# Kernel tuning notes

Measured on AMD Instinct MI355X. Metric: run time of the kernel, lower is better.

The kernel has to match this reference:

```python
import jax, jax.numpy as jnp
import numpy as np

N, E, B = 60000, 360000, 64        # nodes, edges, graphs
IN_DIM, HID, L, NCLS = 256, 512, 3, 1000
EPS = 1e-5                          # BatchNorm1d eps


def setup_inputs() -> dict:
    key = jax.random.key(0)
    ks = jax.random.split(key, 10)
    s = 0.05
    x = jax.random.normal(ks[0], (N, IN_DIM), dtype=jnp.float32)
    edge_index = jax.random.randint(ks[1], (2, E), 0, N, dtype=jnp.int32)
    batch = jnp.sort(jax.random.randint(ks[2], (N,), 0, B, dtype=jnp.int32))
    W_embed = jax.random.normal(ks[3], (IN_DIM, HID), dtype=jnp.float32) * s
    # per-block params (all 3 blocks have identical shapes -> stacked on axis 0)
    W1 = jax.random.normal(ks[4], (L, 2 * HID, HID), dtype=jnp.float32) * s
    b1 = jnp.zeros((L, HID), jnp.float32)
    g1 = jnp.ones((L, HID), jnp.float32)
    be1 = jnp.zeros((L, HID), jnp.float32)
    W2 = jax.random.normal(ks[5], (L, 2 * HID, HID), dtype=jnp.float32) * s
    b2 = jnp.zeros((L, HID), jnp.float32)
    g2 = jnp.ones((L, HID), jnp.float32)
    be2 = jnp.zeros((L, HID), jnp.float32)
    W_att = jax.random.normal(ks[6], (HID, 1), dtype=jnp.float32) * s
    W_read = jax.random.normal(ks[7], (HID, NCLS), dtype=jnp.float32) * s
    return dict(x=x, edge_index=edge_index, batch=batch, W_embed=W_embed,
                W1=W1, b1=b1, g1=g1, be1=be1, W2=W2, b2=b2, g2=g2, be2=be2,
                W_att=W_att, W_read=W_read)


def _segment_mean(vals, idx, num):
    s = jax.ops.segment_sum(vals, idx, num_segments=num)
    c = jax.ops.segment_sum(jnp.ones((vals.shape[0], 1), vals.dtype), idx, num_segments=num)
    return s / jnp.maximum(c, 1.0)


def _bn(h, g, b):  # BatchNorm1d, training-mode batch statistics (biased var)
    m = h.mean(0)
    v = jnp.mean((h - m) ** 2, axis=0)
    return (h - m) * jax.lax.rsqrt(v + EPS) * g + b


def _sage(h, src, dst, W, b):
    # MySAGEConv (position=False -> message = x_j), aggr='mean', concat=True, L2 normalize
    aggr = _segment_mean(h[src], dst, h.shape[0])          # [N, d] mean of neighbor msgs
    out = jnp.concatenate([h, aggr], axis=-1) @ W + b      # [N, 2d] @ [2d, d]
    norm = jnp.linalg.norm(out, axis=-1, keepdims=True)
    return out / jnp.maximum(norm, 1e-12)                  # F.normalize(p=2)


def reference(x, edge_index, batch, W_embed, W1, b1, g1, be1,
              W2, b2, g2, be2, W_att, W_read):
    src, dst = edge_index[0], edge_index[1]
    h = x @ W_embed
    for l in range(L):  # MySAGEConvBlock, gcn_num=2, has_linear_in_block=False
        identity = h
        out = jax.nn.relu(_bn(_sage(h, src, dst, W1[l], b1[l]), g1[l], be1[l]))
        out = jax.nn.relu(_bn(_sage(out, src, dst, W2[l], b2[l]), g2[l], be2[l]))
        h = out + identity  # residual (dims match)
    # AttentionClass
    att = jax.nn.sigmoid(h @ W_att)           # [N, 1]
    hx = (att * h + h) * 0.5
    hg = _segment_mean(hx, batch, B)          # global mean pool per graph
    return hg @ W_read                        # [B, 1000] logits
```

## Files before the change

kernel.cpp:

```cpp
#include <hip/hip_runtime.h>
#include <math.h>

#define N_NODES 60000
#define N_EDGES 360000
#define N_GRAPH 64
#define HID 512
#define NCLS 1000
#define BN_EPS 1e-5f
#define NS ((size_t)N_NODES * HID)
#define NB 235

typedef __bf16 bf16x8 __attribute__((ext_vector_type(8)));
typedef float f32x4 __attribute__((ext_vector_type(4)));

static __device__ __forceinline__ unsigned short f2bf(float f) {
  unsigned u = __float_as_uint(f);
  unsigned r = (u + 0x7fffu + ((u >> 16) & 1u)) >> 16;
  return (unsigned short)r;
}
static __device__ __forceinline__ float bfLo(unsigned u) { return __uint_as_float(u << 16); }
static __device__ __forceinline__ float bfHi(unsigned u) { return __uint_as_float(u & 0xffff0000u); }
static __device__ __forceinline__ unsigned packbf(float a, float b) {
  return (unsigned)f2bf(a) | ((unsigned)f2bf(b) << 16);
}

__global__ void write_sentinel(float* out, float v) { out[0] = v; }

__global__ __launch_bounds__(256) void wtrans(const float* __restrict__ W,
                                              unsigned short* __restrict__ Wt,
                                              int K, int N) {
  __shared__ float sh[32][33];
  int kt = blockIdx.x * 32, nt = blockIdx.y * 32;
  int tx = threadIdx.x & 31, ty = threadIdx.x >> 5;
#pragma unroll
  for (int i = 0; i < 4; ++i)
    sh[ty + i * 8][tx] = W[(size_t)(kt + ty + i * 8) * N + nt + tx];
  __syncthreads();
#pragma unroll
  for (int i = 0; i < 4; ++i)
    Wt[(size_t)(nt + ty + i * 8) * K + kt + tx] = f2bf(sh[tx][ty + i * 8]);
}

__global__ __launch_bounds__(256) void count_deg(const int* __restrict__ dst,
                                                 int* __restrict__ deg, int E) {
  int e = blockIdx.x * 256 + threadIdx.x;
  if (e < E) atomicAdd(&deg[dst[e]], 1);
}

__global__ __launch_bounds__(256) void make_invdeg(const int* __restrict__ deg,
                                                   float* __restrict__ inv, int n) {
  int i = blockIdx.x * 256 + threadIdx.x;
  if (i < n) inv[i] = 1.0f / fmaxf((float)deg[i], 1.0f);
}

__global__ __launch_bounds__(256) void scan_part(const int* __restrict__ deg,
                                                 int* __restrict__ bsum, int n) {
  __shared__ int sh[256];
  int i = blockIdx.x * 256 + threadIdx.x;
  sh[threadIdx.x] = (i < n) ? deg[i] : 0;
  __syncthreads();
  for (int off = 128; off; off >>= 1) {
    if (threadIdx.x < off) sh[threadIdx.x] += sh[threadIdx.x + off];
    __syncthreads();
  }
  if (threadIdx.x == 0) bsum[blockIdx.x] = sh[0];
}

__global__ __launch_bounds__(256) void scan_bsums(int* __restrict__ bsum, int nb) {
  __shared__ int sh[256];
  int t = threadIdx.x;
  int v = (t < nb) ? bsum[t] : 0;
  sh[t] = v;
  __syncthreads();
  for (int off = 1; off < 256; off <<= 1) {
    int u = (t >= off) ? sh[t - off] : 0;
    __syncthreads();
    sh[t] += u;
    __syncthreads();
  }
  if (t < nb) bsum[t] = sh[t] - v;
}

__global__ __launch_bounds__(256) void scan_final(const int* __restrict__ deg,
                                                  const int* __restrict__ bsum,
                                                  int* __restrict__ rowptr, int n) {
  __shared__ int sh[256];
  int t = threadIdx.x;
  int i = blockIdx.x * 256 + t;
  int v = (i < n) ? deg[i] : 0;
  sh[t] = v;
  __syncthreads();
  for (int off = 1; off < 256; off <<= 1) {
    int u = (t >= off) ? sh[t - off] : 0;
    __syncthreads();
    sh[t] += u;
    __syncthreads();
  }
  if (i < n) rowptr[i + 1] = bsum[blockIdx.x] + sh[t];
  if (i == 0) rowptr[0] = 0;
}

__global__ __launch_bounds__(256) void fill_csr(const int* __restrict__ src,
                                                const int* __restrict__ dst,
                                                const int* __restrict__ rowptr,
                                                int* __restrict__ fillc,
                                                int* __restrict__ esrc, int E) {
  int e = blockIdx.x * 256 + threadIdx.x;
  if (e < E) {
    int d = dst[e];
    int pos = rowptr[d] + atomicAdd(&fillc[d], 1);
    esrc[pos] = src[e];
  }
}

__global__ __launch_bounds__(256) void bcount(const int* __restrict__ batch,
                                              float* __restrict__ bcnt, int n) {
  __shared__ int h[N_GRAPH];
  if (threadIdx.x < N_GRAPH) h[threadIdx.x] = 0;
  __syncthreads();
  int i = blockIdx.x * 256 + threadIdx.x;
  if (i < n) atomicAdd(&h[batch[i]], 1);
  __syncthreads();
  if (threadIdx.x < N_GRAPH && h[threadIdx.x])
    atomicAdd(&bcnt[threadIdx.x], (float)h[threadIdx.x]);
}

__global__ __launch_bounds__(256) void gemm_glds(
    const unsigned short* __restrict__ Xb, int ldx,
    const unsigned short* __restrict__ Wt, int ldw,
    const float* __restrict__ bias,
    unsigned short* __restrict__ outB, int M) {
  __shared__ __align__(16) unsigned short As[128 * 32];
  __shared__ __align__(16) unsigned short Bs[128 * 32];
  const int tid = threadIdx.x;
  const int bm = blockIdx.x * 128;
  const int bn = blockIdx.y * 128;
  const int wv = tid >> 6, lane = tid & 63;
  const int wm = (wv >> 1) * 64, wn = (wv & 1) * 64;
  const int lm = lane & 15, quad = lane >> 4;
  const int crow = lane >> 2, cseg = (lane & 3) * 8;

  f32x4 zero;
  zero[0] = 0.f; zero[1] = 0.f; zero[2] = 0.f; zero[3] = 0.f;
  f32x4 acc[4][4];
#pragma unroll
  for (int i = 0; i < 4; ++i)
#pragma unroll
    for (int j = 0; j < 4; ++j) acc[i][j] = zero;

  for (int kt = 0; kt < 512; kt += 32) {
    __syncthreads();
#pragma unroll
    for (int r = 0; r < 2; ++r) {
      int chunk = wv + r * 4;
      int row = chunk * 16 + crow;
      const unsigned short* ga = Xb + (size_t)(bm + row) * ldx + kt + cseg;
      const unsigned short* gb = Wt + (size_t)(bn + row) * ldw + kt + cseg;
      __builtin_amdgcn_global_load_lds(
          (const __attribute__((address_space(1))) unsigned int*)ga,
          (__attribute__((address_space(3))) unsigned int*)(As + chunk * 512),
          16, 0, 0);
      __builtin_amdgcn_global_load_lds(
          (const __attribute__((address_space(1))) unsigned int*)gb,
          (__attribute__((address_space(3))) unsigned int*)(Bs + chunk * 512),
          16, 0, 0);
    }
    __syncthreads();
    bf16x8 af[4], bfr[4];
#pragma unroll
    for (int i = 0; i < 4; ++i)
      af[i] = *(const bf16x8*)(As + (wm + i * 16 + lm) * 32 + quad * 8);
#pragma unroll
    for (int j = 0; j < 4; ++j)
      bfr[j] = *(const bf16x8*)(Bs + (wn + j * 16 + lm) * 32 + quad * 8);
#pragma unroll
    for (int i = 0; i < 4; ++i)
#pragma unroll
      for (int j = 0; j < 4; ++j)
        acc[i][j] = __builtin_amdgcn_mfma_f32_16x16x32_bf16(af[i], bfr[j], acc[i][j], 0, 0, 0);
  }

  const int qr = quad * 4;
#pragma unroll
  for (int j = 0; j < 4; ++j) {
    int col = bn + wn + j * 16 + lm;
    float bvv = bias ? bias[col] : 0.f;
#pragma unroll
    for (int i = 0; i < 4; ++i) {
      int rbase = bm + wm + i * 16 + qr;
#pragma unroll
      for (int r = 0; r < 4; ++r) {
        int row = rbase + r;
        if (row < M) outB[(size_t)row * 512 + col] = f2bf(acc[i][j][r] + bvv);
      }
    }
  }
}

__global__ __launch_bounds__(256) void gemm_tiled(
    const float* __restrict__ Xf, int ldx, int K,
    const unsigned short* __restrict__ Wt, int ldw,
    const float* __restrict__ bias,
    unsigned short* __restrict__ outB, int M) {
  __shared__ __align__(16) unsigned short As[128][40];
  __shared__ __align__(16) unsigned short Bs[128][40];
  const int tid = threadIdx.x;
  const int bm = blockIdx.x * 128;
  const int bn = blockIdx.y * 128;
  const int wv = tid >> 6, lane = tid & 63;
  const int wm = (wv >> 1) * 64, wn = (wv & 1) * 64;
  const int lm = lane & 15, quad = lane >> 4, lk = quad * 8;
  const int srow = tid >> 2, sseg = (tid & 3) * 8;

  f32x4 zero;
  zero[0] = 0.f; zero[1] = 0.f; zero[2] = 0.f; zero[3] = 0.f;
  f32x4 acc[4][4];
#pragma unroll
  for (int i = 0; i < 4; ++i)
#pragma unroll
    for (int j = 0; j < 4; ++j) acc[i][j] = zero;

  const int r0 = bm + srow, r1 = bm + 64 + srow;
  for (int kt = 0; kt < K; kt += 32) {
    uint4 a0 = make_uint4(0, 0, 0, 0), a1 = make_uint4(0, 0, 0, 0);
    if (r0 < M) {
      const float* xp = Xf + (size_t)r0 * ldx + kt + sseg;
      float4 f0 = *(const float4*)xp, f1 = *(const float4*)(xp + 4);
      a0.x = packbf(f0.x, f0.y); a0.y = packbf(f0.z, f0.w);
      a0.z = packbf(f1.x, f1.y); a0.w = packbf(f1.z, f1.w);
    }
    if (r1 < M) {
      const float* xp = Xf + (size_t)r1 * ldx + kt + sseg;
      float4 f0 = *(const float4*)xp, f1 = *(const float4*)(xp + 4);
      a1.x = packbf(f0.x, f0.y); a1.y = packbf(f0.z, f0.w);
      a1.z = packbf(f1.x, f1.y); a1.w = packbf(f1.z, f1.w);
    }
    uint4 b0 = *(const uint4*)(Wt + (size_t)(bn + srow) * ldw + kt + sseg);
    uint4 b1 = *(const uint4*)(Wt + (size_t)(bn + 64 + srow) * ldw + kt + sseg);
    __syncthreads();
    *(uint4*)(&As[srow][sseg]) = a0;
    *(uint4*)(&As[srow + 64][sseg]) = a1;
    *(uint4*)(&Bs[srow][sseg]) = b0;
    *(uint4*)(&Bs[srow + 64][sseg]) = b1;
    __syncthreads();
    bf16x8 af[4], bfr[4];
#pragma unroll
    for (int i = 0; i < 4; ++i) af[i] = *(const bf16x8*)(&As[wm + i * 16 + lm][lk]);
#pragma unroll
    for (int j = 0; j < 4; ++j) bfr[j] = *(const bf16x8*)(&Bs[wn + j * 16 + lm][lk]);
#pragma unroll
    for (int i = 0; i < 4; ++i)
#pragma unroll
      for (int j = 0; j < 4; ++j)
        acc[i][j] = __builtin_amdgcn_mfma_f32_16x16x32_bf16(af[i], bfr[j], acc[i][j], 0, 0, 0);
  }

  const int qr = quad * 4;
#pragma unroll
  for (int j = 0; j < 4; ++j) {
    int col = bn + wn + j * 16 + lm;
    float bvv = bias ? bias[col] : 0.f;
#pragma unroll
    for (int i = 0; i < 4; ++i) {
      int rbase = bm + wm + i * 16 + qr;
#pragma unroll
      for (int r = 0; r < 4; ++r) {
        int row = rbase + r;
        if (row < M) outB[(size_t)row * 512 + col] = f2bf(acc[i][j][r] + bvv);
      }
    }
  }
}

__global__ __launch_bounds__(512) void gemm_strip(
    const unsigned short* __restrict__ Xb, int ldx,
    const unsigned short* __restrict__ Wt, int ldw,
    const float* __restrict__ bias,
    unsigned short* __restrict__ outB, int M) {
  __shared__ __align__(16) unsigned short As[64][40];
  const int tid = threadIdx.x;
  const int bm = blockIdx.x * 64;
  const int wv = tid >> 6, lane = tid & 63;
  const int lm = lane & 15, quad = lane >> 4, lk = quad * 8;
  const int cb = wv * 64;
  const int arow = tid >> 3, aseg = (tid & 7) * 4;

  f32x4 zero;
  zero[0] = 0.f; zero[1] = 0.f; zero[2] = 0.f; zero[3] = 0.f;
  f32x4 acc[4][4];
#pragma unroll
  for (int i = 0; i < 4; ++i)
#pragma unroll
    for (int j = 0; j < 4; ++j) acc[i][j] = zero;

  for (int kt = 0; kt < 512; kt += 32) {
    uint2 av = make_uint2(0, 0);
    int gr = bm + arow;
    if (gr < M) av = *(const uint2*)(Xb + (size_t)gr * ldx + kt + aseg);
    bf16x8 bfr[4];
#pragma unroll
    for (int j = 0; j < 4; ++j)
      bfr[j] = *(const bf16x8*)(Wt + (size_t)(cb + j * 16 + lm) * ldw + kt + lk);
    __syncthreads();
    *(uint2*)(&As[arow][aseg]) = av;
    __syncthreads();
    bf16x8 af[4];
#pragma unroll
    for (int i = 0; i < 4; ++i) af[i] = *(const bf16x8*)(&As[i * 16 + lm][lk]);
#pragma unroll
    for (int i = 0; i < 4; ++i)
#pragma unroll
      for (int j = 0; j < 4; ++j)
        acc[i][j] = __builtin_amdgcn_mfma_f32_16x16x32_bf16(af[i], bfr[j], acc[i][j], 0, 0, 0);
  }

  const int qr = quad * 4;
#pragma unroll
  for (int j = 0; j < 4; ++j) {
    int col = cb + j * 16 + lm;
    float bvv = bias ? bias[col] : 0.f;
#pragma unroll
    for (int i = 0; i < 4; ++i) {
      int rbase = bm + i * 16 + qr;
#pragma unroll
      for (int r = 0; r < 4; ++r) {
        int row = rbase + r;
        if (row < M) outB[(size_t)row * 512 + col] = f2bf(acc[i][j][r] + bvv);
      }
    }
  }
}

__global__ __launch_bounds__(256) void aggr_norm(
    unsigned short* __restrict__ Ya, const unsigned short* __restrict__ Yb,
    const int* __restrict__ rowptr, const int* __restrict__ esrc,
    const float* __restrict__ invdeg, int M) {
  int d = blockIdx.x * 4 + (threadIdx.x >> 6);
  int lane = threadIdx.x & 63;
  if (d >= M) return;
  float acc[8] = {0.f, 0.f, 0.f, 0.f, 0.f, 0.f, 0.f, 0.f};
  int beg = rowptr[d], end = rowptr[d + 1];
  for (int e = beg; e < end; ++e) {
    int s = esrc[e];
    uint4 u = *(const uint4*)(Yb + (size_t)s * 512 + lane * 8);
    acc[0] += bfLo(u.x); acc[1] += bfHi(u.x);
    acc[2] += bfLo(u.y); acc[3] += bfHi(u.y);
    acc[4] += bfLo(u.z); acc[5] += bfHi(u.z);
    acc[6] += bfLo(u.w); acc[7] += bfHi(u.w);
  }
  float iv = invdeg[d];
  uint4 a = *(const uint4*)(Ya + (size_t)d * 512 + lane * 8);
  float r0 = bfLo(a.x) + iv * acc[0], r1 = bfHi(a.x) + iv * acc[1];
  float r2 = bfLo(a.y) + iv * acc[2], r3 = bfHi(a.y) + iv * acc[3];
  float r4 = bfLo(a.z) + iv * acc[4], r5 = bfHi(a.z) + iv * acc[5];
  float r6 = bfLo(a.w) + iv * acc[6], r7 = bfHi(a.w) + iv * acc[7];
  float ss = r0 * r0 + r1 * r1 + r2 * r2 + r3 * r3
           + r4 * r4 + r5 * r5 + r6 * r6 + r7 * r7;
#pragma unroll
  for (int o = 32; o; o >>= 1) ss += __shfl_xor(ss, o, 64);
  float inv = 1.0f / fmaxf(sqrtf(ss), 1e-12f);
  uint4 o4;
  o4.x = packbf(r0 * inv, r1 * inv);
  o4.y = packbf(r2 * inv, r3 * inv);
  o4.z = packbf(r4 * inv, r5 * inv);
  o4.w = packbf(r6 * inv, r7 * inv);
  *(uint4*)(Ya + (size_t)d * 512 + lane * 8) = o4;
}

__global__ __launch_bounds__(256) void bn_stats(const unsigned short* __restrict__ T,
                                                int M, float* __restrict__ sums) {
  const int t = threadIdx.x;
  int r0 = blockIdx.x * 128;
  int rend = min(r0 + 128, M);
  float s0 = 0.f, q0 = 0.f, s1 = 0.f, q1 = 0.f;
  for (int r = r0; r < rend; ++r) {
    float a = __uint_as_float((unsigned)T[(size_t)r * 512 + t] << 16);
    float b = __uint_as_float((unsigned)T[(size_t)r * 512 + t + 256] << 16);
    s0 += a; q0 += a * a; s1 += b; q1 += b * b;
  }
  atomicAdd(&sums[t], s0);
  atomicAdd(&sums[t + 256], s1);
  atomicAdd(&sums[512 + t], q0);
  atomicAdd(&sums[512 + t + 256], q1);
}

__global__ __launch_bounds__(256) void bn_apply(const unsigned short* __restrict__ U,
                                                unsigned short* __restrict__ H,
                                                const float* __restrict__ sums,
                                                const float* __restrict__ g,
                                                const float* __restrict__ be,
                                                int M, int residual) {
  size_t i2 = (size_t)blockIdx.x * 256 + threadIdx.x;
  if (i2 >= NS / 2) return;
  int c = ((int)(i2 & 255)) * 2;
  float invM = 1.0f / (float)M;
  float m0 = sums[c] * invM, m1 = sums[c + 1] * invM;
  float v0 = sums[512 + c] * invM - m0 * m0;
  float v1 = sums[512 + c + 1] * invM - m1 * m1;
  float k0 = rsqrtf(v0 + BN_EPS) * g[c], k1 = rsqrtf(v1 + BN_EPS) * g[c + 1];
  unsigned u = ((const unsigned*)U)[i2];
  float x0 = fmaxf((bfLo(u) - m0) * k0 + be[c], 0.f);
  float x1 = fmaxf((bfHi(u) - m1) * k1 + be[c + 1], 0.f);
  if (residual) {
    unsigned hv = ((const unsigned*)H)[i2];
    x0 += bfLo(hv);
    x1 += bfHi(hv);
  }
  ((unsigned*)H)[i2] = packbf(x0, x1);
}

#define NPB 64
__global__ __launch_bounds__(256) void att_pool2(const unsigned short* __restrict__ H,
                                                 const int* __restrict__ batch,
                                                 const float* __restrict__ Watt,
                                                 float* __restrict__ hg, int M) {
  __shared__ float fsh[NPB];
  __shared__ int bsh[NPB];
  const int tid = threadIdx.x;
  const int base = blockIdx.x * NPB;
  if (tid < NPB) bsh[tid] = (base + tid < M) ? batch[base + tid] : -1;
  const int wv = tid >> 6, lane = tid & 63;
  float4 wa0 = *(const float4*)(Watt + lane * 8);
  float4 wa1 = *(const float4*)(Watt + lane * 8 + 4);
  __syncthreads();
  for (int i = wv; i < NPB; i += 4) {
    int node = base + i;
    float dot = 0.f;
    if (node < M) {
      uint4 u = *(const uint4*)(H + (size_t)node * 512 + lane * 8);
      dot = bfLo(u.x) * wa0.x + bfHi(u.x) * wa0.y
          + bfLo(u.y) * wa0.z + bfHi(u.y) * wa0.w
          + bfLo(u.z) * wa1.x + bfHi(u.z) * wa1.y
          + bfLo(u.w) * wa1.z + bfHi(u.w) * wa1.w;
    }
#pragma unroll
    for (int o = 32; o; o >>= 1) dot += __shfl_xor(dot, o, 64);
    if (lane == 0) fsh[i] = 0.5f * (1.0f + 1.0f / (1.0f + expf(-dot)));
  }
  __syncthreads();
  float a0 = 0.f, a1 = 0.f;
  int cur = bsh[0];
  for (int i = 0; i < NPB; ++i) {
    int node = base + i;
    if (node >= M) break;
    int b = bsh[i];
    if (b != cur) {
      atomicAdd(&hg[(size_t)cur * 512 + tid * 2], a0);
      atomicAdd(&hg[(size_t)cur * 512 + tid * 2 + 1], a1);
      a0 = a1 = 0.f;
      cur = b;
    }
    unsigned u = *(const unsigned*)(H + (size_t)node * 512 + tid * 2);
    float f = fsh[i];
    a0 += bfLo(u) * f;
    a1 += bfHi(u) * f;
  }
  if (cur >= 0) {
    atomicAdd(&hg[(size_t)cur * 512 + tid * 2], a0);
    atomicAdd(&hg[(size_t)cur * 512 + tid * 2 + 1], a1);
  }
}

__global__ __launch_bounds__(256) void readout(const float* __restrict__ hg,
                                               const float* __restrict__ bcnt,
                                               const float* __restrict__ Wr,
                                               float* __restrict__ out) {
  __shared__ float sh[HID];
  int g = blockIdx.x;
  int n = blockIdx.y * 256 + threadIdx.x;
  float inv = 1.0f / fmaxf(bcnt[g], 1.0f);
  for (int k = threadIdx.x; k < HID; k += 256) sh[k] = hg[(size_t)g * HID + k] * inv;
  __syncthreads();
  if (n < NCLS) {
    float acc = 0.f;
    for (int k = 0; k < HID; ++k) acc += sh[k] * Wr[(size_t)k * NCLS + n];
    out[(size_t)g * NCLS + n] = acc;
  }
}

extern "C" void kernel_launch(void* const* d_in, const int* in_sizes, int n_in,
                              void* d_out, int out_size, void* d_ws, size_t ws_size,
                              hipStream_t stream) {
  const float* x       = (const float*)d_in[0];
  const int*   ei      = (const int*)d_in[1];
  const int*   batch   = (const int*)d_in[2];
  const float* W_embed = (const float*)d_in[3];
  const float* W1      = (const float*)d_in[4];
  const float* b1      = (const float*)d_in[5];
  const float* g1      = (const float*)d_in[6];
  const float* be1     = (const float*)d_in[7];
  const float* W2      = (const float*)d_in[8];
  const float* b2      = (const float*)d_in[9];
  const float* g2      = (const float*)d_in[10];
  const float* be2     = (const float*)d_in[11];
  const float* Watt    = (const float*)d_in[12];
  const float* Wread   = (const float*)d_in[13];
  float* out = (float*)d_out;

  const int* srcIdx = ei;
  const int* dstIdx = ei + N_EDGES;

  char* p = (char*)d_ws;
  unsigned short* B0 = (unsigned short*)p; p += NS * 2;
  unsigned short* B1 = (unsigned short*)p; p += NS * 2;
  unsigned short* B2 = (unsigned short*)p; p += NS * 2;
  unsigned short* WtE = (unsigned short*)p; p += (size_t)512 * 256 * 2;
  unsigned short* Wt1 = (unsigned short*)p; p += (size_t)3 * 512 * 1024 * 2;
  unsigned short* Wt2 = (unsigned short*)p; p += (size_t)3 * 512 * 1024 * 2;
  float* hg     = (float*)p; p += (size_t)N_GRAPH * HID * 4;
  float* sums   = (float*)p; p += 1024 * 4;
  float* invdeg = (float*)p; p += (size_t)N_NODES * 4;
  float* bcnt   = (float*)p; p += 256;
  int* deg      = (int*)p;   p += (size_t)N_NODES * 4;
  int* fillc    = (int*)p;   p += (size_t)N_NODES * 4;
  int* esrc     = (int*)p;   p += (size_t)N_EDGES * 4;
  int* rowptr   = (int*)p;   p += (size_t)(N_NODES + 1) * 4;
  int* bsum     = (int*)p;   p += (size_t)NB * 4;
  size_t need3 = (size_t)(p - (char*)d_ws);
  if (ws_size < need3) {
    write_sentinel<<<1, 1, 0, stream>>>(out, (float)need3);
    return;
  }
  unsigned short* B3 = nullptr;
  if (ws_size >= need3 + NS * 2) B3 = (unsigned short*)((char*)d_ws + need3);

  wtrans<<<dim3(8, 16), 256, 0, stream>>>(W_embed, WtE, 256, 512);
  for (int l = 0; l < 3; ++l) {
    wtrans<<<dim3(32, 16), 256, 0, stream>>>(W1 + (size_t)l * 1024 * 512,
                                             Wt1 + (size_t)l * 512 * 1024, 1024, 512);
    wtrans<<<dim3(32, 16), 256, 0, stream>>>(W2 + (size_t)l * 1024 * 512,
                                             Wt2 + (size_t)l * 512 * 1024, 1024, 512);
  }

  hipMemsetAsync(deg, 0, N_NODES * sizeof(int), stream);
  hipMemsetAsync(fillc, 0, N_NODES * sizeof(int), stream);
  count_deg<<<(N_EDGES + 255) / 256, 256, 0, stream>>>(dstIdx, deg, N_EDGES);
  make_invdeg<<<(N_NODES + 255) / 256, 256, 0, stream>>>(deg, invdeg, N_NODES);
  scan_part<<<NB, 256, 0, stream>>>(deg, bsum, N_NODES);
  scan_bsums<<<1, 256, 0, stream>>>(bsum, NB);
  scan_final<<<NB, 256, 0, stream>>>(deg, bsum, rowptr, N_NODES);
  fill_csr<<<(N_EDGES + 255) / 256, 256, 0, stream>>>(srcIdx, dstIdx, rowptr, fillc,
                                                      esrc, N_EDGES);

  const dim3 tgrid((N_NODES + 127) / 128, 4);
  const int sgrid = (N_NODES + 63) / 64;
  const int ngrid = (N_NODES + 3) / 4;
  const int egrid = (int)((NS / 2 + 255) / 256);

  gemm_tiled<<<tgrid, 256, 0, stream>>>(x, 256, 256, WtE, 256, nullptr, B0, N_NODES);

  for (int l = 0; l < 3; ++l) {
    const unsigned short* Wt1l = Wt1 + (size_t)l * 512 * 1024;
    const unsigned short* Wt2l = Wt2 + (size_t)l * 512 * 1024;
    gemm_glds<<<tgrid, 256, 0, stream>>>(B0, 512, Wt1l + 512, 1024,
                                         nullptr, B2, N_NODES);
    gemm_glds<<<tgrid, 256, 0, stream>>>(B0, 512, Wt1l, 1024,
                                         b1 + l * 512, B1, N_NODES);
    aggr_norm<<<ngrid, 256, 0, stream>>>(B1, B2, rowptr, esrc, invdeg, N_NODES);
    hipMemsetAsync(sums, 0, 1024 * sizeof(float), stream);
    bn_stats<<<(N_NODES + 127) / 128, 256, 0, stream>>>(B1, N_NODES, sums);
    bn_apply<<<egrid, 256, 0, stream>>>(B1, B1, sums, g1 + l * 512,
                                        be1 + l * 512, N_NODES, 0);
    gemm_glds<<<tgrid, 256, 0, stream>>>(B1, 512, Wt2l + 512, 1024,
                                         nullptr, B2, N_NODES);
    unsigned short* Ya2 = B3 ? B3 : B1;
    if (B3) {
      gemm_glds<<<tgrid, 256, 0, stream>>>(B1, 512, Wt2l, 1024,
                                           b2 + l * 512, B3, N_NODES);
    } else {
      gemm_strip<<<sgrid, 512, 0, stream>>>(B1, 512, Wt2l, 1024,
                                            b2 + l * 512, B1, N_NODES);
    }
    aggr_norm<<<ngrid, 256, 0, stream>>>(Ya2, B2, rowptr, esrc, invdeg, N_NODES);
    hipMemsetAsync(sums, 0, 1024 * sizeof(float), stream);
    bn_stats<<<(N_NODES + 127) / 128, 256, 0, stream>>>(Ya2, N_NODES, sums);
    bn_apply<<<egrid, 256, 0, stream>>>(Ya2, B0, sums, g2 + l * 512,
                                        be2 + l * 512, N_NODES, 1);
  }

  hipMemsetAsync(hg, 0, (size_t)N_GRAPH * HID * sizeof(float), stream);
  hipMemsetAsync(bcnt, 0, N_GRAPH * sizeof(float), stream);
  bcount<<<NB, 256, 0, stream>>>(batch, bcnt, N_NODES);
  att_pool2<<<(N_NODES + NPB - 1) / NPB, 256, 0, stream>>>(B0, batch, Watt, hg, N_NODES);
  readout<<<dim3(N_GRAPH, 4), 256, 0, stream>>>(hg, bcnt, Wread, out);
}
```

Before: 2.211 ms.

## Remap gemm_glds blocks per XCD, fix LDS fragment layout, stage output via LDS

Replaces the 2D grid of gemm_glds with a 1D grid that spreads contiguous 128-row strips across the eight XCDs, so the four column tiles of a strip share one XCD's L2. It changes the global_load_lds lane-to-row mapping so each 16-row chunk is stored in MFMA fragment order, letting each lane read its fragment as one contiguous 16-byte LDS access. The epilogue now stages bf16 results in an LDS tile and writes full 16-byte rows to global memory instead of scattered 2-byte stores. This adds LDS use and two extra barrier phases per block. The grid of 1888 blocks includes 12 idle blocks that return immediately, and the workspace threshold for B3 is made slightly stricter.

```diff
diff --git a/kernel.cpp b/kernel.cpp
--- a/kernel.cpp
+++ b/kernel.cpp
@@ -9,6 +9,7 @@
 #define BN_EPS 1e-5f
 #define NS ((size_t)N_NODES * HID)
 #define NB 235
+#define STRIPS 469
 
 typedef __bf16 bf16x8 __attribute__((ext_vector_type(8)));
 typedef float f32x4 __attribute__((ext_vector_type(4)));
@@ -132,13 +133,18 @@
     unsigned short* __restrict__ outB, int M) {
   __shared__ __align__(16) unsigned short As[128 * 32];
   __shared__ __align__(16) unsigned short Bs[128 * 32];
+  __shared__ __align__(16) unsigned short Cs[64][136];
   const int tid = threadIdx.x;
-  const int bm = blockIdx.x * 128;
-  const int bn = blockIdx.y * 128;
+  const int L = blockIdx.x;
+  const int xcd = L & 7, li = L >> 3;
+  const int strip = xcd * 59 + (li >> 2);
+  if (strip >= STRIPS) return;
+  const int bm = strip * 128;
+  const int bn = (li & 3) * 128;
   const int wv = tid >> 6, lane = tid & 63;
   const int wm = (wv >> 1) * 64, wn = (wv & 1) * 64;
   const int lm = lane & 15, quad = lane >> 4;
-  const int crow = lane >> 2, cseg = (lane & 3) * 8;
+  const int grow = lane & 15, gseg = (lane >> 4) * 8;
 
   f32x4 zero;
   zero[0] = 0.f; zero[1] = 0.f; zero[2] = 0.f; zero[3] = 0.f;
@@ -153,9 +159,9 @@
 #pragma unroll
     for (int r = 0; r < 2; ++r) {
       int chunk = wv + r * 4;
-      int row = chunk * 16 + crow;
-      const unsigned short* ga = Xb + (size_t)(bm + row) * ldx + kt + cseg;
-      const unsigned short* gb = Wt + (size_t)(bn + row) * ldw + kt + cseg;
+      int row = chunk * 16 + grow;
+      const unsigned short* ga = Xb + (size_t)(bm + row) * ldx + kt + gseg;
+      const unsigned short* gb = Wt + (size_t)(bn + row) * ldw + kt + gseg;
       __builtin_amdgcn_global_load_lds(
           (const __attribute__((address_space(1))) unsigned int*)ga,
           (__attribute__((address_space(3))) unsigned int*)(As + chunk * 512),
@@ -169,10 +175,10 @@
     bf16x8 af[4], bfr[4];
 #pragma unroll
     for (int i = 0; i < 4; ++i)
-      af[i] = *(const bf16x8*)(As + (wm + i * 16 + lm) * 32 + quad * 8);
+      af[i] = *(const bf16x8*)(As + (wm / 16 + i) * 512 + lane * 8);
 #pragma unroll
     for (int j = 0; j < 4; ++j)
-      bfr[j] = *(const bf16x8*)(Bs + (wn + j * 16 + lm) * 32 + quad * 8);
+      bfr[j] = *(const bf16x8*)(Bs + (wn / 16 + j) * 512 + lane * 8);
 #pragma unroll
     for (int i = 0; i < 4; ++i)
 #pragma unroll
@@ -181,18 +187,29 @@
   }
 
   const int qr = quad * 4;
-#pragma unroll
-  for (int j = 0; j < 4; ++j) {
-    int col = bn + wn + j * 16 + lm;
-    float bvv = bias ? bias[col] : 0.f;
-#pragma unroll
-    for (int i = 0; i < 4; ++i) {
-      int rbase = bm + wm + i * 16 + qr;
-#pragma unroll
-      for (int r = 0; r < 4; ++r) {
-        int row = rbase + r;
-        if (row < M) outB[(size_t)row * 512 + col] = f2bf(acc[i][j][r] + bvv);
+  const int rl = tid >> 4, seg = (tid & 15) * 8;
+#pragma unroll
+  for (int p = 0; p < 2; ++p) {
+    __syncthreads();
+    if ((wv >> 1) == p) {
+#pragma unroll
+      for (int j = 0; j < 4; ++j) {
+        int col = wn + j * 16 + lm;
+        float bvv = bias ? bias[bn + col] : 0.f;
+#pragma unroll
+        for (int i = 0; i < 4; ++i)
+#pragma unroll
+          for (int r = 0; r < 4; ++r)
+            Cs[i * 16 + qr + r][col] = f2bf(acc[i][j][r] + bvv);
       }
+    }
+    __syncthreads();
+#pragma unroll
+    for (int pass = 0; pass < 4; ++pass) {
+      int row = bm + p * 64 + pass * 16 + rl;
+      if (row < M)
+        *(uint4*)(outB + (size_t)row * 512 + bn + seg) =
+            *(const uint4*)(&Cs[pass * 16 + rl][seg]);
     }
   }
 }
@@ -522,7 +539,7 @@
     return;
   }
   unsigned short* B3 = nullptr;
-  if (ws_size >= need3 + NS * 2) B3 = (unsigned short*)((char*)d_ws + need3);
+  if (ws_size >= need3 + NS * 2 + 65536) B3 = (unsigned short*)((char*)d_ws + need3);
 
   wtrans<<<dim3(8, 16), 256, 0, stream>>>(W_embed, WtE, 256, 512);
   for (int l = 0; l < 3; ++l) {
@@ -542,6 +559,7 @@
   fill_csr<<<(N_EDGES + 255) / 256, 256, 0, stream>>>(srcIdx, dstIdx, rowptr, fillc,
                                                       esrc, N_EDGES);
 
+  const int ggrid = 8 * 59 * 4;
   const dim3 tgrid((N_NODES + 127) / 128, 4);
   const int sgrid = (N_NODES + 63) / 64;
   const int ngrid = (N_NODES + 3) / 4;
@@ -552,20 +570,20 @@
   for (int l = 0; l < 3; ++l) {
     const unsigned short* Wt1l = Wt1 + (size_t)l * 512 * 1024;
     const unsigned short* Wt2l = Wt2 + (size_t)l * 512 * 1024;
-    gemm_glds<<<tgrid, 256, 0, stream>>>(B0, 512, Wt1l + 512, 1024,
+    gemm_glds<<<ggrid, 256, 0, stream>>>(B0, 512, Wt1l + 512, 1024,
                                          nullptr, B2, N_NODES);
-    gemm_glds<<<tgrid, 256, 0, stream>>>(B0, 512, Wt1l, 1024,
+    gemm_glds<<<ggrid, 256, 0, stream>>>(B0, 512, Wt1l, 1024,
                                          b1 + l * 512, B1, N_NODES);
     aggr_norm<<<ngrid, 256, 0, stream>>>(B1, B2, rowptr, esrc, invdeg, N_NODES);
     hipMemsetAsync(sums, 0, 1024 * sizeof(float), stream);
     bn_stats<<<(N_NODES + 127) / 128, 256, 0, stream>>>(B1, N_NODES, sums);
     bn_apply<<<egrid, 256, 0, stream>>>(B1, B1, sums, g1 + l * 512,
                                         be1 + l * 512, N_NODES, 0);
-    gemm_glds<<<tgrid, 256, 0, stream>>>(B1, 512, Wt2l + 512, 1024,
+    gemm_glds<<<ggrid, 256, 0, stream>>>(B1, 512, Wt2l + 512, 1024,
                                          nullptr, B2, N_NODES);
     unsigned short* Ya2 = B3 ? B3 : B1;
     if (B3) {
-      gemm_glds<<<tgrid, 256, 0, stream>>>(B1, 512, Wt2l, 1024,
+      gemm_glds<<<ggrid, 256, 0, stream>>>(B1, 512, Wt2l, 1024,
                                            b2 + l * 512, B3, N_NODES);
     } else {
       gemm_strip<<<sgrid, 512, 0, stream>>>(B1, 512, Wt2l, 1024,
```

Measured after the change: 2.087 ms. 1.06x faster.
